# Kernel optimization log

Hardware: AMD Instinct MI355X
Metric: run time of the kernel (lower is better)

The kernel has to match this reference:

```python
import jax, jax.numpy as jnp
import numpy as np

N = 100000
E = 1600000
F_IN, F_HID, F_OUT = 128, 64, 1


def setup_inputs() -> dict:
    key = jax.random.key(0)
    ks = jax.random.split(key, 8)
    x = jax.random.normal(ks[0], (N, F_IN), dtype=jnp.float32)
    edge_index = jax.random.randint(ks[1], (2, E), 0, N, dtype=jnp.int64)
    def glorot(k, fan_in, fan_out):
        scale = jnp.sqrt(2.0 / (fan_in + fan_out)).astype(jnp.float32)
        return jax.random.normal(k, (fan_in, fan_out), dtype=jnp.float32) * scale
    W1 = glorot(ks[2], F_IN, F_HID); b1 = jnp.zeros((F_HID,), jnp.float32)
    W2 = glorot(ks[3], F_HID, F_HID); b2 = jnp.zeros((F_HID,), jnp.float32)
    W3 = glorot(ks[4], F_HID, F_OUT); b3 = jnp.zeros((F_OUT,), jnp.float32)
    return {"x": x, "W1": W1, "b1": b1, "W2": W2, "b2": b2, "W3": W3, "b3": b3, "edge_index": edge_index}


def _gcn_norm(edge_index, n):
    # add self-loops, symmetric D^{-1/2} (A+I) D^{-1/2} normalization (PyG GCNConv default)
    loop = jnp.arange(n, dtype=edge_index.dtype)
    src = jnp.concatenate([edge_index[0], loop])
    dst = jnp.concatenate([edge_index[1], loop])
    deg = jax.ops.segment_sum(jnp.ones_like(src, dtype=jnp.float32), dst, num_segments=n)
    dis = jnp.where(deg > 0, jax.lax.rsqrt(jnp.maximum(deg, 1.0)), 0.0)
    norm = dis[src] * dis[dst]  # [E+N]
    return src, dst, norm


def _gcn_conv(h, W, b, src, dst, norm, n):
    h = h @ W                                   # [N, f_out]
    msg = h[src] * norm[:, None]                # gather + scale, [E+N, f_out]
    out = jax.ops.segment_sum(msg, dst, num_segments=n)  # scatter-add
    return out + b


def reference(x, W1, b1, W2, b2, W3, b3, edge_index):
    n = x.shape[0]
    src, dst, norm = _gcn_norm(edge_index, n)
    h = jax.nn.relu(_gcn_conv(x, W1, b1, src, dst, norm, n))
    h = jax.nn.relu(_gcn_conv(h, W2, b2, src, dst, norm, n))
    h = _gcn_conv(h, W3, b3, src, dst, norm, n)
    return jax.nn.sigmoid(h)
```

## Files before the change

### kernel.cpp

```cpp
#include <hip/hip_runtime.h>
#include <math.h>

#define NN 100000
#define NE 1600000
#define NSHARD 4
#define SHARD_W (NN / NSHARD)
#define NCHUNK 64
#define CHUNK_E (NE / NCHUNK)
#define CHUNK_I4 (CHUNK_E / 4)

typedef __attribute__((ext_vector_type(8))) short bf16x8;
typedef __attribute__((ext_vector_type(4))) float f32x4;
typedef __attribute__((ext_vector_type(2))) float f32x2;

__device__ inline unsigned f2bf(float f) {
    unsigned u = __float_as_uint(f);
    u += 0x7FFFu + ((u >> 16) & 1u);
    return u >> 16;
}
__device__ inline float bflo(unsigned v) { return __uint_as_float(v << 16); }
__device__ inline float bfhi(unsigned v) { return __uint_as_float(v & 0xFFFF0000u); }
__device__ inline f32x2 bfpair(unsigned u) {
    f32x2 r;
    r.x = __uint_as_float(u << 16);
    r.y = __uint_as_float(u & 0xFFFF0000u);
    return r;
}

__global__ __launch_bounds__(256) void k_cnt(const int4* __restrict__ dst4,
                                             unsigned char* __restrict__ cnt,
                                             unsigned char* __restrict__ lrank) {
    __shared__ __align__(16) unsigned ldeg[SHARD_W];
    int t = threadIdx.x;
    int shard = blockIdx.x & (NSHARD - 1);
    int b = blockIdx.x >> 2;
    int lo = shard * SHARD_W;
    uint4 z4 = make_uint4(0u, 0u, 0u, 0u);
    for (int i = t; i < SHARD_W / 4; i += 256) ((uint4*)ldeg)[i] = z4;
    __syncthreads();
    const int4* p = dst4 + b * CHUNK_I4;
    unsigned char* lr = lrank + b * CHUNK_E;
#pragma unroll 4
    for (int j = t; j < CHUNK_I4; j += 256) {
        int4 d = p[j];
        unsigned ex = (unsigned)(d.x - lo);
        unsigned ey = (unsigned)(d.y - lo);
        unsigned ez = (unsigned)(d.z - lo);
        unsigned ew = (unsigned)(d.w - lo);
        if (ex < SHARD_W) lr[4 * j + 0] = (unsigned char)atomicAdd(&ldeg[ex], 1u);
        if (ey < SHARD_W) lr[4 * j + 1] = (unsigned char)atomicAdd(&ldeg[ey], 1u);
        if (ez < SHARD_W) lr[4 * j + 2] = (unsigned char)atomicAdd(&ldeg[ez], 1u);
        if (ew < SHARD_W) lr[4 * j + 3] = (unsigned char)atomicAdd(&ldeg[ew], 1u);
    }
    __syncthreads();
    unsigned* cb32 = (unsigned*)cnt + b * (NN / 4) + shard * (SHARD_W / 4);
    for (int i = t; i < SHARD_W / 4; i += 256) {
        uint4 v = *(const uint4*)&ldeg[4 * i];
        cb32[i] = (v.x & 255u) | ((v.y & 255u) << 8) | ((v.z & 255u) << 16)
                | ((v.w & 255u) << 24);
    }
}

__global__ __launch_bounds__(256) void k_blkscan(unsigned char* __restrict__ cnt,
                                                 int* __restrict__ deg,
                                                 int* __restrict__ bsums) {
    __shared__ int s[256];
    int i = blockIdx.x * 256 + threadIdx.x;
    int total = 0;
    if (i < NN) {
        unsigned a = 0;
#pragma unroll
        for (int b = 0; b < NCHUNK; ++b) {
            unsigned v = cnt[b * NN + i];
            cnt[b * NN + i] = (unsigned char)a;
            a += v;
        }
        deg[i] = (int)a;
        total = (int)a;
    }
    s[threadIdx.x] = total;
    __syncthreads();
    for (int off = 128; off > 0; off >>= 1) {
        if (threadIdx.x < off) s[threadIdx.x] += s[threadIdx.x + off];
        __syncthreads();
    }
    if (threadIdx.x == 0) bsums[blockIdx.x] = s[0];
}

__global__ void k_rowptr(const int* __restrict__ deg, const int* __restrict__ bsums,
                         int* __restrict__ rowptr, float* __restrict__ dis) {
    __shared__ int sbase[256];
    __shared__ int s[256];
    int t = threadIdx.x;
    int bid = blockIdx.x;
    int v = (t < bid) ? bsums[t] : 0;
    if (t + 256 < bid) v += bsums[t + 256];
    sbase[t] = v;
    __syncthreads();
    for (int off = 128; off > 0; off >>= 1) {
        if (t < off) sbase[t] += sbase[t + off];
        __syncthreads();
    }
    int base = sbase[0];
    int i = bid * 256 + t;
    int d = (i < NN) ? deg[i] : 0;
    s[t] = d;
    __syncthreads();
    for (int off = 1; off < 256; off <<= 1) {
        int x = (t >= off) ? s[t - off] : 0;
        __syncthreads();
        s[t] += x;
        __syncthreads();
    }
    if (i < NN) {
        rowptr[i] = base + s[t] - d;
        dis[i] = rsqrtf((float)(d + 1));
    }
    if (i == 0) rowptr[NN] = NE;
}

__global__ __launch_bounds__(256) void k_build_csr(
    const int4* __restrict__ src4, const int4* __restrict__ dst4,
    const unsigned char* __restrict__ blkoff, const unsigned* __restrict__ lr4,
    const int* __restrict__ rowptr, int* __restrict__ csr) {
    int shard = blockIdx.x & (NSHARD - 1);
    int bsh = blockIdx.x >> 2;
    int stride = (gridDim.x >> 2) * 256;
    int lo = shard * SHARD_W;
    const int NE4 = NE / 4;
    for (int i = bsh * 256 + threadIdx.x; i < NE4; i += stride) {
        int4 d = dst4[i];
        int4 s = src4[i];
        unsigned lr = lr4[i];
        const unsigned char* off = blkoff + (i / CHUNK_I4) * NN;
        unsigned ex = (unsigned)(d.x - lo);
        unsigned ey = (unsigned)(d.y - lo);
        unsigned ez = (unsigned)(d.z - lo);
        unsigned ew = (unsigned)(d.w - lo);
        if (ex < SHARD_W) csr[rowptr[d.x] + off[d.x] + (lr & 255u)] = s.x;
        if (ey < SHARD_W) csr[rowptr[d.y] + off[d.y] + ((lr >> 8) & 255u)] = s.y;
        if (ez < SHARD_W) csr[rowptr[d.z] + off[d.z] + ((lr >> 16) & 255u)] = s.z;
        if (ew < SHARD_W) csr[rowptr[d.w] + off[d.w] + (lr >> 24)] = s.w;
    }
}

#define XS_LD 136
__global__ __launch_bounds__(256) void k_gemm1(
    const float* __restrict__ x, const float* __restrict__ W,
    const float* __restrict__ dis, unsigned short* __restrict__ tsb) {
    __shared__ unsigned short xs[64 * XS_LD];
    __shared__ unsigned short wt[64 * XS_LD];
    int t = threadIdx.x;
    int row0 = blockIdx.x * 64;
    for (int i = t; i < 64 * 64; i += 256) {
        int n = i & 63, k2 = i >> 6;
        float w0 = W[(2 * k2) * 64 + n];
        float w1 = W[(2 * k2 + 1) * 64 + n];
        *(unsigned*)&wt[n * XS_LD + 2 * k2] = f2bf(w0) | (f2bf(w1) << 16);
    }
    for (int i = t; i < 64 * 32; i += 256) {
        int r = i >> 5, c4 = i & 31;
        int gr = row0 + r;
        uint2 p = {0u, 0u};
        if (gr < NN) {
            float4 v = *(const float4*)&x[gr * 128 + 4 * c4];
            p.x = f2bf(v.x) | (f2bf(v.y) << 16);
            p.y = f2bf(v.z) | (f2bf(v.w) << 16);
        }
        *(uint2*)&xs[r * XS_LD + 4 * c4] = p;
    }
    __syncthreads();
    int w = t >> 6, l = t & 63;
    int lm = l & 15, lg = l >> 4;
    const unsigned short* ap = &xs[(16 * w + lm) * XS_LD + 8 * lg];
    const unsigned short* bp = &wt[lm * XS_LD + 8 * lg];
    f32x4 acc0 = {0, 0, 0, 0}, acc1 = {0, 0, 0, 0}, acc2 = {0, 0, 0, 0}, acc3 = {0, 0, 0, 0};
#pragma unroll
    for (int kb = 0; kb < 4; ++kb) {
        bf16x8 a  = *(const bf16x8*)(ap + 32 * kb);
        bf16x8 b0 = *(const bf16x8*)(bp + 32 * kb);
        bf16x8 b1 = *(const bf16x8*)(bp + 16 * XS_LD + 32 * kb);
        bf16x8 b2 = *(const bf16x8*)(bp + 32 * XS_LD + 32 * kb);
        bf16x8 b3 = *(const bf16x8*)(bp + 48 * XS_LD + 32 * kb);
        acc0 = __builtin_amdgcn_mfma_f32_16x16x32_bf16(a, b0, acc0, 0, 0, 0);
        acc1 = __builtin_amdgcn_mfma_f32_16x16x32_bf16(a, b1, acc1, 0, 0, 0);
        acc2 = __builtin_amdgcn_mfma_f32_16x16x32_bf16(a, b2, acc2, 0, 0, 0);
        acc3 = __builtin_amdgcn_mfma_f32_16x16x32_bf16(a, b3, acc3, 0, 0, 0);
    }
    int rbase = row0 + 16 * w + 4 * lg;
#pragma unroll
    for (int r = 0; r < 4; ++r) {
        int row = rbase + r;
        if (row < NN) {
            float dv = dis[row];
            unsigned short* o = &tsb[row * 64 + lm];
            o[0]  = (unsigned short)f2bf(acc0[r] * dv);
            o[16] = (unsigned short)f2bf(acc1[r] * dv);
            o[32] = (unsigned short)f2bf(acc2[r] * dv);
            o[48] = (unsigned short)f2bf(acc3[r] * dv);
        }
    }
}

#define HS_LD 72
__global__ __launch_bounds__(256) void k_gemm2(
    const unsigned short* __restrict__ hb, const float* __restrict__ W,
    const float* __restrict__ dis, unsigned short* __restrict__ tsb) {
    __shared__ unsigned short hs[64 * HS_LD];
    __shared__ unsigned short wh[64 * HS_LD];
    __shared__ unsigned short wl[64 * HS_LD];
    int t = threadIdx.x;
    int row0 = blockIdx.x * 64;
    for (int i = t; i < 64 * 32; i += 256) {
        int n = i & 63, k2 = i >> 6;
        float w0 = W[(2 * k2) * 64 + n];
        float w1 = W[(2 * k2 + 1) * 64 + n];
        unsigned h0 = f2bf(w0), h1 = f2bf(w1);
        *(unsigned*)&wh[n * HS_LD + 2 * k2] = h0 | (h1 << 16);
        float r0 = w0 - bflo(h0), r1 = w1 - bflo(h1);
        *(unsigned*)&wl[n * HS_LD + 2 * k2] = f2bf(r0) | (f2bf(r1) << 16);
    }
    const uint4* h4 = (const uint4*)hb;
    for (int i = t; i < 64 * 8; i += 256) {
        int r = i >> 3, c8 = i & 7;
        int gr = row0 + r;
        uint4 v = (gr < NN) ? h4[gr * 8 + c8] : make_uint4(0u, 0u, 0u, 0u);
        *(uint4*)&hs[r * HS_LD + 8 * c8] = v;
    }
    __syncthreads();
    int w = t >> 6, l = t & 63;
    int lm = l & 15, lg = l >> 4;
    const unsigned short* ap = &hs[(16 * w + lm) * HS_LD + 8 * lg];
    const unsigned short* bh = &wh[lm * HS_LD + 8 * lg];
    const unsigned short* bl = &wl[lm * HS_LD + 8 * lg];
    f32x4 acc0 = {0, 0, 0, 0}, acc1 = {0, 0, 0, 0}, acc2 = {0, 0, 0, 0}, acc3 = {0, 0, 0, 0};
#pragma unroll
    for (int kb = 0; kb < 2; ++kb) {
        bf16x8 a  = *(const bf16x8*)(ap + 32 * kb);
        bf16x8 h0 = *(const bf16x8*)(bh + 32 * kb);
        bf16x8 h1 = *(const bf16x8*)(bh + 16 * HS_LD + 32 * kb);
        bf16x8 h2 = *(const bf16x8*)(bh + 32 * HS_LD + 32 * kb);
        bf16x8 h3 = *(const bf16x8*)(bh + 48 * HS_LD + 32 * kb);
        bf16x8 l0 = *(const bf16x8*)(bl + 32 * kb);
        bf16x8 l1 = *(const bf16x8*)(bl + 16 * HS_LD + 32 * kb);
        bf16x8 l2 = *(const bf16x8*)(bl + 32 * HS_LD + 32 * kb);
        bf16x8 l3 = *(const bf16x8*)(bl + 48 * HS_LD + 32 * kb);
        acc0 = __builtin_amdgcn_mfma_f32_16x16x32_bf16(a, h0, acc0, 0, 0, 0);
        acc1 = __builtin_amdgcn_mfma_f32_16x16x32_bf16(a, h1, acc1, 0, 0, 0);
        acc2 = __builtin_amdgcn_mfma_f32_16x16x32_bf16(a, h2, acc2, 0, 0, 0);
        acc3 = __builtin_amdgcn_mfma_f32_16x16x32_bf16(a, h3, acc3, 0, 0, 0);
        acc0 = __builtin_amdgcn_mfma_f32_16x16x32_bf16(a, l0, acc0, 0, 0, 0);
        acc1 = __builtin_amdgcn_mfma_f32_16x16x32_bf16(a, l1, acc1, 0, 0, 0);
        acc2 = __builtin_amdgcn_mfma_f32_16x16x32_bf16(a, l2, acc2, 0, 0, 0);
        acc3 = __builtin_amdgcn_mfma_f32_16x16x32_bf16(a, l3, acc3, 0, 0, 0);
    }
    int rbase = row0 + 16 * w + 4 * lg;
#pragma unroll
    for (int r = 0; r < 4; ++r) {
        int row = rbase + r;
        if (row < NN) {
            float dv = dis[row];
            unsigned short* o = &tsb[row * 64 + lm];
            o[0]  = (unsigned short)f2bf(acc0[r] * dv);
            o[16] = (unsigned short)f2bf(acc1[r] * dv);
            o[32] = (unsigned short)f2bf(acc2[r] * dv);
            o[48] = (unsigned short)f2bf(acc3[r] * dv);
        }
    }
}

#define AGG_BLOCKS 2048
template <bool FUSE3>
__global__ __launch_bounds__(256) void k_agg_relu(
    const unsigned short* __restrict__ tsb, const int* __restrict__ rowptr,
    const int* __restrict__ csr, const float* __restrict__ dis,
    const float* __restrict__ b, const float* __restrict__ W3,
    unsigned short* __restrict__ hb, float* __restrict__ t3) {
    int wid = blockIdx.x * 4 + (threadIdx.x >> 6);
    const int nwaves = AGG_BLOCKS * 4;
    int lane = threadIdx.x & 63;
    int half = lane >> 5;
    int oct = (lane >> 3) & 3;
    int fl = lane & 7;
    const uint4* ts128 = (const uint4*)tsb;
    for (int base = wid * 2; base < NN; base += nwaves * 2) {
        int node = base + half;
        bool valid = node < NN;
        f32x2 a0 = {0.f, 0.f}, a1 = {0.f, 0.f}, a2 = {0.f, 0.f}, a3 = {0.f, 0.f};
        if (valid) {
            if (oct == 0) {
                uint4 v = ts128[node * 8 + fl];
                a0 += bfpair(v.x); a1 += bfpair(v.y); a2 += bfpair(v.z); a3 += bfpair(v.w);
            }
            int e = rowptr[node] + oct, end = rowptr[node + 1];
            for (; e + 12 < end; e += 16) {
                int s0 = csr[e];
                int s1 = csr[e + 4];
                int s2 = csr[e + 8];
                int s3 = csr[e + 12];
                uint4 v0 = ts128[s0 * 8 + fl];
                uint4 v1 = ts128[s1 * 8 + fl];
                uint4 v2 = ts128[s2 * 8 + fl];
                uint4 v3 = ts128[s3 * 8 + fl];
                a0 += bfpair(v0.x); a1 += bfpair(v0.y); a2 += bfpair(v0.z); a3 += bfpair(v0.w);
                a0 += bfpair(v1.x); a1 += bfpair(v1.y); a2 += bfpair(v1.z); a3 += bfpair(v1.w);
                a0 += bfpair(v2.x); a1 += bfpair(v2.y); a2 += bfpair(v2.z); a3 += bfpair(v2.w);
                a0 += bfpair(v3.x); a1 += bfpair(v3.y); a2 += bfpair(v3.z); a3 += bfpair(v3.w);
            }
            for (; e < end; e += 4) {
                uint4 v = ts128[csr[e] * 8 + fl];
                a0 += bfpair(v.x); a1 += bfpair(v.y); a2 += bfpair(v.z); a3 += bfpair(v.w);
            }
        }
#pragma unroll
        for (int off = 8; off <= 16; off <<= 1) {
            a0.x += __shfl_xor(a0.x, off); a0.y += __shfl_xor(a0.y, off);
            a1.x += __shfl_xor(a1.x, off); a1.y += __shfl_xor(a1.y, off);
            a2.x += __shfl_xor(a2.x, off); a2.y += __shfl_xor(a2.y, off);
            a3.x += __shfl_xor(a3.x, off); a3.y += __shfl_xor(a3.y, off);
        }
        if (valid && oct == 0) {
            float dv = dis[node];
            float v0 = fmaxf(a0.x * dv + b[8 * fl + 0], 0.f);
            float v1 = fmaxf(a0.y * dv + b[8 * fl + 1], 0.f);
            float v2 = fmaxf(a1.x * dv + b[8 * fl + 2], 0.f);
            float v3 = fmaxf(a1.y * dv + b[8 * fl + 3], 0.f);
            float v4 = fmaxf(a2.x * dv + b[8 * fl + 4], 0.f);
            float v5 = fmaxf(a2.y * dv + b[8 * fl + 5], 0.f);
            float v6 = fmaxf(a3.x * dv + b[8 * fl + 6], 0.f);
            float v7 = fmaxf(a3.y * dv + b[8 * fl + 7], 0.f);
            if (FUSE3) {
                float part = v0 * W3[8 * fl + 0] + v1 * W3[8 * fl + 1]
                           + v2 * W3[8 * fl + 2] + v3 * W3[8 * fl + 3]
                           + v4 * W3[8 * fl + 4] + v5 * W3[8 * fl + 5]
                           + v6 * W3[8 * fl + 6] + v7 * W3[8 * fl + 7];
                part += __shfl_xor(part, 1);
                part += __shfl_xor(part, 2);
                part += __shfl_xor(part, 4);
                if (fl == 0) t3[node] = part * dv;
            } else {
                uint4 p;
                p.x = f2bf(v0) | (f2bf(v1) << 16);
                p.y = f2bf(v2) | (f2bf(v3) << 16);
                p.z = f2bf(v4) | (f2bf(v5) << 16);
                p.w = f2bf(v6) | (f2bf(v7) << 16);
                ((uint4*)hb)[node * 8 + fl] = p;
            }
        }
    }
}

__global__ void k_out(const float* __restrict__ t3, const int* __restrict__ rowptr,
                      const int* __restrict__ csr, const float* __restrict__ dis,
                      const float* __restrict__ b3, float* __restrict__ out) {
    int i = blockIdx.x * 256 + threadIdx.x;
    if (i >= NN) return;
    float acc = t3[i];
    float acc1 = 0.f, acc2 = 0.f, acc3 = 0.f;
    int e = rowptr[i], end = rowptr[i + 1];
    for (; e + 4 <= end; e += 4) {
        acc += t3[csr[e]];
        acc1 += t3[csr[e + 1]];
        acc2 += t3[csr[e + 2]];
        acc3 += t3[csr[e + 3]];
    }
    for (; e < end; ++e) acc += t3[csr[e]];
    float z = ((acc + acc1) + (acc2 + acc3)) * dis[i] + b3[0];
    out[i] = 1.f / (1.f + __expf(-z));
}

extern "C" void kernel_launch(void* const* d_in, const int* in_sizes, int n_in,
                              void* d_out, int out_size, void* d_ws, size_t ws_size,
                              hipStream_t stream) {
    const float* x  = (const float*)d_in[0];
    const float* W1 = (const float*)d_in[1];
    const float* b1 = (const float*)d_in[2];
    const float* W2 = (const float*)d_in[3];
    const float* b2 = (const float*)d_in[4];
    const float* W3 = (const float*)d_in[5];
    const float* b3 = (const float*)d_in[6];
    const int*   ei = (const int*)d_in[7];
    const int* src = ei;
    const int* dst = ei + NE;
    float* out = (float*)d_out;

    unsigned short* TSB = (unsigned short*)d_ws;
    unsigned short* HB  = TSB + (size_t)NN * 64;
    float* dis    = (float*)(HB + (size_t)NN * 64);
    float* t3     = dis + NN;
    int*   deg    = (int*)(t3 + NN);
    int*   rowptr = deg + NN;
    int*   bsums  = rowptr + NN + 8;
    int*   csr    = bsums + 512;
    unsigned char* lrank = (unsigned char*)TSB;
    unsigned char* cnt   = (unsigned char*)HB;

    const int nbN = (NN + 255) / 256;
    const int nbG = (NN + 63) / 64;

    k_cnt<<<NSHARD * NCHUNK, 256, 0, stream>>>((const int4*)dst, cnt, lrank);
    k_blkscan<<<nbN, 256, 0, stream>>>(cnt, deg, bsums);
    k_rowptr<<<nbN, 256, 0, stream>>>(deg, bsums, rowptr, dis);
    k_build_csr<<<2048, 256, 0, stream>>>((const int4*)src, (const int4*)dst,
                                          cnt, (const unsigned*)lrank, rowptr, csr);

    k_gemm1<<<nbG, 256, 0, stream>>>(x, W1, dis, TSB);
    k_agg_relu<false><<<AGG_BLOCKS, 256, 0, stream>>>(TSB, rowptr, csr, dis, b1, W3, HB, t3);

    k_gemm2<<<nbG, 256, 0, stream>>>(HB, W2, dis, TSB);
    k_agg_relu<true><<<AGG_BLOCKS, 256, 0, stream>>>(TSB, rowptr, csr, dis, b2, W3, HB, t3);

    k_out<<<nbN, 256, 0, stream>>>(t3, rowptr, csr, dis, b3, out);
}
```

Measured before the change: 264.7 us.

## Merge CSR build and first GEMM into one interleaved kernel launch

Combines the CSR scatter kernel and the first-layer GEMM into a single launch, interleaving their blocks 4:3 so the latency-bound scatter and the compute-bound GEMM run concurrently on the GPU. The lrank buffer is moved out of TSB into HB, because TSB is now written by the GEMM while the scatter is still reading lrank. This saves one launch and overlaps two independent phases. In exchange, the GEMM blocks' shared-memory footprint applies to the scatter blocks too, which may lower occupancy for the scatter part.

```diff
diff --git a/kernel.cpp b/kernel.cpp
--- a/kernel.cpp
+++ b/kernel.cpp
@@ -8,6 +8,8 @@
 #define NCHUNK 64
 #define CHUNK_E (NE / NCHUNK)
 #define CHUNK_I4 (CHUNK_E / 4)
+#define NCSRB 2048
+#define NG1B ((NN + 63) / 64)
 
 typedef __attribute__((ext_vector_type(8))) short bf16x8;
 typedef __attribute__((ext_vector_type(4))) float f32x4;
@@ -119,39 +121,44 @@
     if (i == 0) rowptr[NN] = NE;
 }
 
-__global__ __launch_bounds__(256) void k_build_csr(
+#define XS_LD 136
+__global__ __launch_bounds__(256) void k_csr_gemm1(
     const int4* __restrict__ src4, const int4* __restrict__ dst4,
     const unsigned char* __restrict__ blkoff, const unsigned* __restrict__ lr4,
-    const int* __restrict__ rowptr, int* __restrict__ csr) {
-    int shard = blockIdx.x & (NSHARD - 1);
-    int bsh = blockIdx.x >> 2;
-    int stride = (gridDim.x >> 2) * 256;
-    int lo = shard * SHARD_W;
-    const int NE4 = NE / 4;
-    for (int i = bsh * 256 + threadIdx.x; i < NE4; i += stride) {
-        int4 d = dst4[i];
-        int4 s = src4[i];
-        unsigned lr = lr4[i];
-        const unsigned char* off = blkoff + (i / CHUNK_I4) * NN;
-        unsigned ex = (unsigned)(d.x - lo);
-        unsigned ey = (unsigned)(d.y - lo);
-        unsigned ez = (unsigned)(d.z - lo);
-        unsigned ew = (unsigned)(d.w - lo);
-        if (ex < SHARD_W) csr[rowptr[d.x] + off[d.x] + (lr & 255u)] = s.x;
-        if (ey < SHARD_W) csr[rowptr[d.y] + off[d.y] + ((lr >> 8) & 255u)] = s.y;
-        if (ez < SHARD_W) csr[rowptr[d.z] + off[d.z] + ((lr >> 16) & 255u)] = s.z;
-        if (ew < SHARD_W) csr[rowptr[d.w] + off[d.w] + (lr >> 24)] = s.w;
-    }
-}
-
-#define XS_LD 136
-__global__ __launch_bounds__(256) void k_gemm1(
+    const int* __restrict__ rowptr, int* __restrict__ csr,
     const float* __restrict__ x, const float* __restrict__ W,
     const float* __restrict__ dis, unsigned short* __restrict__ tsb) {
+    int t = threadIdx.x;
+    int grp = blockIdx.x / 7, rem = blockIdx.x % 7;
+    if (rem < 4) {
+        int ci = grp * 4 + rem;
+        if (ci >= NCSRB) return;
+        int shard = ci & (NSHARD - 1);
+        int bsh = ci >> 2;
+        int stride = (NCSRB >> 2) * 256;
+        int lo = shard * SHARD_W;
+        const int NE4 = NE / 4;
+        for (int i = bsh * 256 + t; i < NE4; i += stride) {
+            int4 d = dst4[i];
+            int4 s = src4[i];
+            unsigned lr = lr4[i];
+            const unsigned char* off = blkoff + (i / CHUNK_I4) * NN;
+            unsigned ex = (unsigned)(d.x - lo);
+            unsigned ey = (unsigned)(d.y - lo);
+            unsigned ez = (unsigned)(d.z - lo);
+            unsigned ew = (unsigned)(d.w - lo);
+            if (ex < SHARD_W) csr[rowptr[d.x] + off[d.x] + (lr & 255u)] = s.x;
+            if (ey < SHARD_W) csr[rowptr[d.y] + off[d.y] + ((lr >> 8) & 255u)] = s.y;
+            if (ez < SHARD_W) csr[rowptr[d.z] + off[d.z] + ((lr >> 16) & 255u)] = s.z;
+            if (ew < SHARD_W) csr[rowptr[d.w] + off[d.w] + (lr >> 24)] = s.w;
+        }
+        return;
+    }
+    int gi = grp * 3 + (rem - 4);
+    if (gi >= NG1B) return;
     __shared__ unsigned short xs[64 * XS_LD];
     __shared__ unsigned short wt[64 * XS_LD];
-    int t = threadIdx.x;
-    int row0 = blockIdx.x * 64;
+    int row0 = gi * 64;
     for (int i = t; i < 64 * 64; i += 256) {
         int n = i & 63, k2 = i >> 6;
         float w0 = W[(2 * k2) * 64 + n];
@@ -392,22 +399,25 @@
     int*   rowptr = deg + NN;
     int*   bsums  = rowptr + NN + 8;
     int*   csr    = bsums + 512;
-    unsigned char* lrank = (unsigned char*)TSB;
     unsigned char* cnt   = (unsigned char*)HB;
+    unsigned char* lrank = (unsigned char*)HB + (size_t)NCHUNK * NN;
 
     const int nbN = (NN + 255) / 256;
     const int nbG = (NN + 63) / 64;
+    const int nbMerged = 7 * 523;
 
     k_cnt<<<NSHARD * NCHUNK, 256, 0, stream>>>((const int4*)dst, cnt, lrank);
     k_blkscan<<<nbN, 256, 0, stream>>>(cnt, deg, bsums);
     k_rowptr<<<nbN, 256, 0, stream>>>(deg, bsums, rowptr, dis);
-    k_build_csr<<<2048, 256, 0, stream>>>((const int4*)src, (const int4*)dst,
-                                          cnt, (const unsigned*)lrank, rowptr, csr);
-
-    k_gemm1<<<nbG, 256, 0, stream>>>(x, W1, dis, TSB);
+
+    k_csr_gemm1<<<nbMerged, 256, 0, stream>>>((const int4*)src, (const int4*)dst,
+                                              cnt, (const unsigned*)lrank, rowptr, csr,
+                                              x, W1, dis, TSB);
+
     k_agg_relu<false><<<AGG_BLOCKS, 256, 0, stream>>>(TSB, rowptr, csr, dis, b1, W3, HB, t3);
 
     k_gemm2<<<nbG, 256, 0, stream>>>(HB, W2, dis, TSB);
+
     k_agg_relu<true><<<AGG_BLOCKS, 256, 0, stream>>>(TSB, rowptr, csr, dis, b2, W3, HB, t3);
 
     k_out<<<nbN, 256, 0, stream>>>(t3, rowptr, csr, dis, b3, out);
```

Result: slower. 275.1 us (+3.9%).
